# Kernel optimization log

Hardware: AMD Instinct MI355X
Metric: run time of the kernel (lower is better)

Reference implementation:

```python
import jax, jax.numpy as jnp
import numpy as np

N = 100000
F_IN = 128
E = 1_600_000
NEG_SLOPE = 0.2  # PyG GATConv default negative_slope


def _seg_sum(v, idx, n):
    return jax.ops.segment_sum(v, idx, num_segments=n)


def gcn_conv(x, W, b, src, dst, n):
    # PyG GCNConv: D^{-1/2} (A + I) D^{-1/2} X W + b (self loops already in src/dst)
    h = x @ W
    deg = _seg_sum(jnp.ones(src.shape, h.dtype), dst, n)
    dinv = jnp.where(deg > 0, jax.lax.rsqrt(deg), 0.0)
    norm = dinv[src] * dinv[dst]  # [E]
    return _seg_sum(h[src] * norm[:, None], dst, n) + b


def gat_conv(x, W, a_src, a_dst, b, src, dst, n, heads, out_ch):
    # PyG GATConv (concat=True), eval mode (dropout inactive)
    h = (x @ W).reshape(n, heads, out_ch)          # [n,H,C]
    s = jnp.einsum('nhc,hc->nh', h, a_src)          # per-node src score
    t = jnp.einsum('nhc,hc->nh', h, a_dst)          # per-node dst score
    e = jax.nn.leaky_relu(s[src] + t[dst], NEG_SLOPE)  # [E,H]
    m = jax.ops.segment_max(e, dst, num_segments=n)    # stable segment softmax
    m = jnp.where(jnp.isfinite(m), m, 0.0)
    p = jnp.exp(e - m[dst])
    denom = _seg_sum(p, dst, n)
    alpha = p / (denom[dst] + 1e-16)                 # [E,H]
    out = _seg_sum(h[src] * alpha[:, :, None], dst, n)  # [n,H,C]
    return out.reshape(n, heads * out_ch) + b


def setup_inputs():
    key = jax.random.key(0)
    ks = jax.random.split(key, 24)
    x = jax.random.normal(ks[0], (N, F_IN), jnp.float32) * 0.1
    half = N // 2
    # one-hot user/item type flags read by forward (x[:,0]==1 / x[:,1]==1)
    x = x.at[:, 0].set(0.0).at[:, 1].set(0.0)
    x = x.at[:half, 0].set(1.0).at[half:, 1].set(1.0)
    src = jax.random.randint(ks[1], (E,), 0, N, dtype=jnp.int32)
    dst = jax.random.randint(ks[2], (E,), 0, N, dtype=jnp.int32)
    edge_index = jnp.stack([src, dst])

    def p(k, shape):
        return jax.random.normal(k, shape, jnp.float32) * 0.1

    inp = {"x": x, "edge_index": edge_index,
           "gcn_w": p(ks[3], (F_IN, 16)), "gcn_b": jnp.zeros((16,), jnp.float32)}
    dims = [(16, 16, 8), (128, 16, 8), (128, 16, 8), (128, 2, 1)]
    for i, (fi, fo, h) in enumerate(dims, start=1):
        inp[f"g{i}_w"] = p(ks[3 + 4 * i], (fi, h * fo))
        inp[f"g{i}_as"] = p(ks[4 + 4 * i], (h, fo))
        inp[f"g{i}_ad"] = p(ks[5 + 4 * i], (h, fo))
        inp[f"g{i}_b"] = jnp.zeros((h * fo,), jnp.float32)
    return inp


def reference(x, edge_index, gcn_w, gcn_b,
              g1_w, g1_as, g1_ad, g1_b,
              g2_w, g2_as, g2_ad, g2_b,
              g3_w, g3_as, g3_ad, g3_b,
              g4_w, g4_as, g4_ad, g4_b):
    n = x.shape[0]
    loops = jnp.arange(n, dtype=edge_index.dtype)  # self loops (added by GCN/GAT layers)
    src = jnp.concatenate([edge_index[0], loops])
    dst = jnp.concatenate([edge_index[1], loops])
    h = jax.nn.elu(gcn_conv(x, gcn_w, gcn_b, src, dst, n))
    h = jax.nn.elu(gat_conv(h, g1_w, g1_as, g1_ad, g1_b, src, dst, n, 8, 16))
    h = jax.nn.elu(gat_conv(h, g2_w, g2_as, g2_ad, g2_b, src, dst, n, 8, 16))
    h = jax.nn.elu(gat_conv(h, g3_w, g3_as, g3_ad, g3_b, src, dst, n, 8, 16))
    h = jax.nn.elu(gat_conv(h, g4_w, g4_as, g4_ad, g4_b, src, dst, n, 1, 2))  # [n,2]
    half = n // 2  # users are rows [:half], items rows [half:]
    out = jnp.concatenate([h[:half], h[half:]], axis=1)  # [half,4]
    return jax.nn.log_softmax(out, axis=1)
```

## Files before the change

### kernel.cpp

```cpp
#include <hip/hip_runtime.h>
#include <cstddef>
#include <cstdint>

#define NN 100000
#define NPAD 100032
#define NE 1600000
#define ET (NE + NN)
#define ETP_MAX (ET + 8 * NN)
#define HALFN (NN / 2)
#define NEG_SLOPE 0.2f
#define SCB 1024
#define RP 8
#define RNODES (NN / RP)
#define CHUNK 8192

typedef __attribute__((ext_vector_type(8))) short short8v;
typedef __attribute__((ext_vector_type(4))) float float4v;
typedef __attribute__((ext_vector_type(2))) float float2v;

__device__ __forceinline__ float lrelu(float x) { return x > 0.f ? x : NEG_SLOPE * x; }

__device__ __forceinline__ uint16_t f2bf(float f) {
  uint32_t u = __float_as_uint(f);
  uint32_t r = u + 0x7fffu + ((u >> 16) & 1u);
  return (uint16_t)(r >> 16);
}
__device__ __forceinline__ float bflo(uint32_t u) { return __uint_as_float(u << 16); }
__device__ __forceinline__ float bfhi(uint32_t u) { return __uint_as_float(u & 0xffff0000u); }

template<int K, int M>
__launch_bounds__(256)
__global__ void gemm4_kernel(const float* __restrict__ X, const float* __restrict__ W,
                             float* __restrict__ Y, int n) {
  constexpr int CG = M / 4;
  constexpr int RG = 256 / CG;
  constexpr int RPT = 2;
  constexpr int RT = RG * RPT;
  constexpr int KP = K + 1;
  __shared__ __align__(16) float sW[K * M];
  __shared__ float sX[RT * KP];
  for (int i = threadIdx.x; i < K * M; i += 256) sW[i] = W[i];
  const int jg = threadIdx.x % CG;
  const int rg = threadIdx.x / CG;
  const int r0 = rg * RPT;
  for (int base = blockIdx.x * RT; base < n; base += gridDim.x * RT) {
    __syncthreads();
    const int nrows = (n - base) < RT ? (n - base) : RT;
    for (int i = threadIdx.x; i < nrows * K; i += 256) {
      int r = i / K, c = i - r * K;
      sX[r * KP + c] = X[(size_t)base * K + i];
    }
    __syncthreads();
    float acc[RPT][4];
    #pragma unroll
    for (int rr = 0; rr < RPT; ++rr) acc[rr][0] = acc[rr][1] = acc[rr][2] = acc[rr][3] = 0.f;
    #pragma unroll 4
    for (int k = 0; k < K; ++k) {
      const float4 w = *(const float4*)&sW[k * M + jg * 4];
      #pragma unroll
      for (int rr = 0; rr < RPT; ++rr) {
        const float xv = sX[(r0 + rr) * KP + k];
        acc[rr][0] = fmaf(xv, w.x, acc[rr][0]);
        acc[rr][1] = fmaf(xv, w.y, acc[rr][1]);
        acc[rr][2] = fmaf(xv, w.z, acc[rr][2]);
        acc[rr][3] = fmaf(xv, w.w, acc[rr][3]);
      }
    }
    #pragma unroll
    for (int rr = 0; rr < RPT; ++rr) {
      if (r0 + rr < nrows) {
        float4 o = make_float4(acc[rr][0], acc[rr][1], acc[rr][2], acc[rr][3]);
        *(float4*)&Y[(size_t)(base + r0 + rr) * M + jg * 4] = o;
      }
    }
  }
}

template<int KB>
__launch_bounds__(256)
__global__ void wpack_kernel(const float* __restrict__ W, uint16_t* __restrict__ wp,
                             int Kreal) {
  int tid = blockIdx.x * 256 + threadIdx.x;
  if (tid >= KB * 8 * 64) return;
  int lane = tid & 63;
  int ctkb = tid >> 6;
  int kb = ctkb % KB, ct = ctkb / KB;
  int nc = ct * 16 + (lane & 15);
  int k0 = kb * 32 + (lane >> 4) * 8;
  ushort4 o0, o1;
  uint16_t v[8];
  #pragma unroll
  for (int j = 0; j < 8; ++j) {
    int k = k0 + j;
    v[j] = (k < Kreal) ? f2bf(W[(size_t)k * 128 + nc]) : (uint16_t)0;
  }
  o0.x = v[0]; o0.y = v[1]; o0.z = v[2]; o0.w = v[3];
  o1.x = v[4]; o1.y = v[5]; o1.z = v[6]; o1.w = v[7];
  *(ushort4*)&wp[(size_t)tid * 8] = o0;
  *(ushort4*)&wp[(size_t)tid * 8 + 4] = o1;
}

template<int KB, int XS>
__launch_bounds__(256)
__global__ void gemm_mfma_kernel(const uint16_t* __restrict__ X,
                                 const uint16_t* __restrict__ wp,
                                 const float* __restrict__ aS, const float* __restrict__ aD,
                                 uint16_t* __restrict__ Y,
                                 float* __restrict__ S, float* __restrict__ T, int n) {
  __shared__ float sC[4][16 * 136];
  const int wv = threadIdx.x >> 6;
  const int lane = threadIdx.x & 63;
  const int rowbase = blockIdx.x * 64 + wv * 16;
  int arow = rowbase + (lane & 15);
  if (arow >= n) arow = n - 1;
  const uint16_t* xp = X + (size_t)arow * XS + ((lane >> 4) * 8);
  short8v a[KB];
  #pragma unroll
  for (int kb = 0; kb < KB; ++kb) a[kb] = *(const short8v*)(xp + kb * 32);
  #pragma unroll
  for (int ct = 0; ct < 8; ++ct) {
    float4v acc = {0.f, 0.f, 0.f, 0.f};
    #pragma unroll
    for (int kb = 0; kb < KB; ++kb) {
      short8v b = *(const short8v*)&wp[(size_t)((ct * KB + kb) * 64 + lane) * 8];
      acc = __builtin_amdgcn_mfma_f32_16x16x32_bf16(a[kb], b, acc, 0, 0, 0);
    }
    #pragma unroll
    for (int r = 0; r < 4; ++r)
      sC[wv][((lane >> 4) * 4 + r) * 136 + ct * 16 + (lane & 15)] = acc[r];
  }
  #pragma unroll
  for (int t = 0; t < 4; ++t) {
    int idx = t * 64 + lane;
    int row = idx >> 4;
    int c8 = idx & 15;
    const float* pr = &sC[wv][row * 136 + c8 * 8];
    float4 lo = *(const float4*)pr;
    float4 hi = *(const float4*)(pr + 4);
    uint4 o;
    o.x = (uint32_t)f2bf(lo.x) | ((uint32_t)f2bf(lo.y) << 16);
    o.y = (uint32_t)f2bf(lo.z) | ((uint32_t)f2bf(lo.w) << 16);
    o.z = (uint32_t)f2bf(hi.x) | ((uint32_t)f2bf(hi.y) << 16);
    o.w = (uint32_t)f2bf(hi.z) | ((uint32_t)f2bf(hi.w) << 16);
    *(uint4*)&Y[(size_t)(rowbase + row) * 128 + c8 * 8] = o;
  }
  {
    int r = lane & 15;
    int hg = lane >> 4;
    int node = rowbase + r;
    if (node < n) {
      #pragma unroll
      for (int hh = 0; hh < 2; ++hh) {
        int h = hg * 2 + hh;
        float sv = 0.f, tv = 0.f;
        #pragma unroll
        for (int c = 0; c < 16; ++c) {
          float v = sC[wv][r * 136 + h * 16 + c];
          sv = fmaf(v, aS[h * 16 + c], sv);
          tv = fmaf(v, aD[h * 16 + c], tv);
        }
        S[(size_t)node * 8 + h] = sv;
        T[(size_t)node * 8 + h] = tv;
      }
    }
  }
}

template<int K, int M, int ROWS>
__launch_bounds__(256)
__global__ void gemm_s_kernel(const uint16_t* __restrict__ Xb, const float* __restrict__ W,
                              float* __restrict__ Y, int n) {
  constexpr int KP = K + 1;
  __shared__ float sW[K * M];
  __shared__ float sX[ROWS * KP];
  for (int i = threadIdx.x; i < K * M; i += 256) sW[i] = W[i];
  for (int base = blockIdx.x * ROWS; base < n; base += gridDim.x * ROWS) {
    __syncthreads();
    const int nrows = (n - base) < ROWS ? (n - base) : ROWS;
    for (int i = threadIdx.x; i < nrows * (K / 4); i += 256) {
      int r = i / (K / 4), c = i - r * (K / 4);
      uint2 u = *(const uint2*)&Xb[(size_t)(base + r) * K + c * 4];
      sX[r * KP + c * 4 + 0] = bflo(u.x);
      sX[r * KP + c * 4 + 1] = bfhi(u.x);
      sX[r * KP + c * 4 + 2] = bflo(u.y);
      sX[r * KP + c * 4 + 3] = bfhi(u.y);
    }
    __syncthreads();
    for (int o = threadIdx.x; o < nrows * M; o += 256) {
      int r = o / M, j = o - r * M;
      float a = 0.f;
      #pragma unroll
      for (int k = 0; k < K; ++k) a = fmaf(sX[r * KP + k], sW[k * M + j], a);
      Y[(size_t)(base + r) * M + j] = a;
    }
  }
}

__global__ void spad_kernel(float* __restrict__ S, float* __restrict__ T) {
  if (threadIdx.x < 8) {
    S[(size_t)NN * 8 + threadIdx.x] = -1e30f;
    T[(size_t)NN * 8 + threadIdx.x] = 0.f;
  }
}

template<int H, int C>
__launch_bounds__(256)
__global__ void score_kernel(const float* __restrict__ Hm,
                             const float* __restrict__ aS, const float* __restrict__ aD,
                             float* __restrict__ S, float* __restrict__ T, int n) {
  int idx = blockIdx.x * 256 + threadIdx.x;
  int tot = n * H;
  if (idx >= tot + H) return;
  if (idx >= tot) { S[idx] = -1e30f; T[idx] = 0.f; return; }
  int h = idx & (H - 1);
  const float* hp = Hm + (size_t)idx * C;
  float s = 0.f, t = 0.f;
  #pragma unroll
  for (int c = 0; c < C; ++c) {
    float v = hp[c];
    s = fmaf(v, aS[h * C + c], s);
    t = fmaf(v, aD[h * C + c], t);
  }
  S[idx] = s;
  T[idx] = t;
}

__launch_bounds__(256)
__global__ void rank_kernel(const int* __restrict__ edst, int* __restrict__ cursor,
                            int* __restrict__ rank) {
  int e = blockIdx.x * 256 + threadIdx.x;
  if (e >= ET) return;
  int dn = e < NE ? edst[e] : e - NE;
  rank[e] = atomicAdd(&cursor[dn], 1);
}

__device__ __forceinline__ int pad8(int d) { return (d + 7) & ~7; }

__launch_bounds__(256)
__global__ void scan1_kernel(const int* __restrict__ degi, int* __restrict__ rowptr,
                             int* __restrict__ bsums) {
  __shared__ int sd[256];
  int t = threadIdx.x;
  int base = blockIdx.x * SCB + t * 4;
  int v0 = base + 0 < NN ? pad8(degi[base + 0]) : 0;
  int v1 = base + 1 < NN ? pad8(degi[base + 1]) : 0;
  int v2 = base + 2 < NN ? pad8(degi[base + 2]) : 0;
  int v3 = base + 3 < NN ? pad8(degi[base + 3]) : 0;
  int s = v0 + v1 + v2 + v3;
  sd[t] = s;
  __syncthreads();
  for (int off = 1; off < 256; off <<= 1) {
    int x = (t >= off) ? sd[t - off] : 0;
    __syncthreads();
    sd[t] += x;
    __syncthreads();
  }
  int excl = sd[t] - s;
  if (t == 255) bsums[blockIdx.x] = sd[255];
  if (base + 0 < NN) rowptr[base + 0] = excl;
  excl += v0;
  if (base + 1 < NN) rowptr[base + 1] = excl;
  excl += v1;
  if (base + 2 < NN) rowptr[base + 2] = excl;
  excl += v2;
  if (base + 3 < NN) rowptr[base + 3] = excl;
}

__launch_bounds__(256)
__global__ void scan2_kernel(int* __restrict__ bsums, int nb) {
  __shared__ int sd[256];
  int t = threadIdx.x;
  int v = t < nb ? bsums[t] : 0;
  sd[t] = v;
  __syncthreads();
  for (int off = 1; off < 256; off <<= 1) {
    int x = (t >= off) ? sd[t - off] : 0;
    __syncthreads();
    sd[t] += x;
    __syncthreads();
  }
  if (t < nb) bsums[t] = sd[t] - v;
  if (t == nb - 1) bsums[nb] = sd[t];
}

__launch_bounds__(256)
__global__ void scan3_kernel(int* __restrict__ rowptr, const int* __restrict__ bsums, int nb) {
  int i = blockIdx.x * 256 + threadIdx.x;
  if (i < NN) rowptr[i] += bsums[i / SCB];
  if (i == 0) rowptr[NN] = bsums[nb];
}

__launch_bounds__(256)
__global__ void dinv_kernel(const int* __restrict__ deg, float* __restrict__ dinv) {
  int i = blockIdx.x * 256 + threadIdx.x;
  if (i > NN) return;
  if (i == NN) { dinv[i] = 0.f; return; }
  int d = deg[i];
  dinv[i] = d > 0 ? rsqrtf((float)d) : 0.f;
}

__launch_bounds__(256)
__global__ void csr_fill_kernel(int* __restrict__ csr) {
  int i = blockIdx.x * 256 + threadIdx.x;
  if (i < ETP_MAX) csr[i] = NN;
}

__launch_bounds__(256)
__global__ void scatter_part_kernel(const int* __restrict__ esrc, const int* __restrict__ edst,
                                    const int* __restrict__ rowptr, const int* __restrict__ rank,
                                    int* __restrict__ csr_src) {
  int p = blockIdx.x & (RP - 1);
  int c = blockIdx.x >> 3;
  int lo = p * RNODES, hi = lo + RNODES;
  int e0 = c * CHUNK;
  int e1 = e0 + CHUNK < ET ? e0 + CHUNK : ET;
  for (int e = e0 + threadIdx.x; e < e1; e += 256) {
    int dn = e < NE ? edst[e] : e - NE;
    if (dn >= lo && dn < hi) {
      int sn = e < NE ? esrc[e] : e - NE;
      csr_src[rowptr[dn] + rank[e]] = sn;
    }
  }
}

__launch_bounds__(256)
__global__ void fused_gat_kernel(const int* __restrict__ rowptr, const int* __restrict__ csr,
                                 const float* __restrict__ S, const float* __restrict__ T,
                                 const uint16_t* __restrict__ Hm, const float* __restrict__ bias,
                                 uint16_t* __restrict__ Outb) {
  const int lane = threadIdx.x & 63;
  const int d = (blockIdx.x * 256 + threadIdx.x) >> 6;
  if (d >= NN) return;
  const int rs = rowptr[d];
  const int deg = rowptr[d + 1] - rs;
  const int eg = lane >> 4;
  const int cl = lane & 15;
  const int hp = cl >> 1;
  const float Th = T[(size_t)d * 8 + hp];
  const char* sb = (const char*)S;
  const char* hb = (const char*)Hm;
  float m = -1e38f;
  float s = 0.f;
  float2v A0 = {0.f, 0.f}, A1 = {0.f, 0.f}, A2 = {0.f, 0.f}, A3 = {0.f, 0.f};
  const uint32_t clo = (uint32_t)(cl << 4);
  const uint32_t hpo = (uint32_t)(hp << 2);
  int iA = rs + eg;
  int snA = csr[iA];
  int snB = csr[iA + 4];
  for (int l0 = 0; l0 < deg; l0 += 8) {
    int snA2 = csr[iA + 8];
    int snB2 = csr[iA + 12];
    uint4 uA = *(const uint4*)(hb + (((uint32_t)snA << 8) + clo));
    uint4 uB = *(const uint4*)(hb + (((uint32_t)snB << 8) + clo));
    float svA = *(const float*)(sb + (((uint32_t)snA << 5) + hpo));
    float svB = *(const float*)(sb + (((uint32_t)snB << 5) + hpo));
    iA += 8;
    float eA = lrelu(svA + Th);
    float eB = lrelu(svB + Th);
    float nm = fmaxf(m, fmaxf(eA, eB));
    if (nm > m) {
      float sc = __expf(m - nm);
      float2v scv = {sc, sc};
      s *= sc;
      A0 *= scv; A1 *= scv; A2 *= scv; A3 *= scv;
      m = nm;
    }
    float pA = __expf(eA - m);
    float pB = __expf(eB - m);
    s += pA + pB;
    float2v ppA = {pA, pA}, ppB = {pB, pB};
    A0 = ppA * (float2v){bflo(uA.x), bfhi(uA.x)} + A0;
    A1 = ppA * (float2v){bflo(uA.y), bfhi(uA.y)} + A1;
    A2 = ppA * (float2v){bflo(uA.z), bfhi(uA.z)} + A2;
    A3 = ppA * (float2v){bflo(uA.w), bfhi(uA.w)} + A3;
    A0 = ppB * (float2v){bflo(uB.x), bfhi(uB.x)} + A0;
    A1 = ppB * (float2v){bflo(uB.y), bfhi(uB.y)} + A1;
    A2 = ppB * (float2v){bflo(uB.z), bfhi(uB.z)} + A2;
    A3 = ppB * (float2v){bflo(uB.w), bfhi(uB.w)} + A3;
    snA = snA2; snB = snB2;
  }
  #pragma unroll
  for (int mask = 16; mask <= 32; mask <<= 1) {
    float om = __shfl_xor(m, mask);
    float os = __shfl_xor(s, mask);
    float o0x = __shfl_xor(A0.x, mask), o0y = __shfl_xor(A0.y, mask);
    float o1x = __shfl_xor(A1.x, mask), o1y = __shfl_xor(A1.y, mask);
    float o2x = __shfl_xor(A2.x, mask), o2y = __shfl_xor(A2.y, mask);
    float o3x = __shfl_xor(A3.x, mask), o3y = __shfl_xor(A3.y, mask);
    float nm = fmaxf(m, om);
    float s1 = __expf(m - nm), s2 = __expf(om - nm);
    s = s * s1 + os * s2;
    A0.x = A0.x * s1 + o0x * s2; A0.y = A0.y * s1 + o0y * s2;
    A1.x = A1.x * s1 + o1x * s2; A1.y = A1.y * s1 + o1y * s2;
    A2.x = A2.x * s1 + o2x * s2; A2.y = A2.y * s1 + o2y * s2;
    A3.x = A3.x * s1 + o3x * s2; A3.y = A3.y * s1 + o3y * s2;
    m = nm;
  }
  if (lane < 16) {
    const float inv = 1.f / (s + 1e-16f);
    float4 b0 = *(const float4*)&bias[cl * 8];
    float4 b1 = *(const float4*)&bias[cl * 8 + 4];
    float v0 = fmaf(A0.x, inv, b0.x), v1 = fmaf(A0.y, inv, b0.y);
    float v2 = fmaf(A1.x, inv, b0.z), v3 = fmaf(A1.y, inv, b0.w);
    float v4 = fmaf(A2.x, inv, b1.x), v5 = fmaf(A2.y, inv, b1.y);
    float v6 = fmaf(A3.x, inv, b1.z), v7 = fmaf(A3.y, inv, b1.w);
    v0 = v0 > 0.f ? v0 : expm1f(v0); v1 = v1 > 0.f ? v1 : expm1f(v1);
    v2 = v2 > 0.f ? v2 : expm1f(v2); v3 = v3 > 0.f ? v3 : expm1f(v3);
    v4 = v4 > 0.f ? v4 : expm1f(v4); v5 = v5 > 0.f ? v5 : expm1f(v5);
    v6 = v6 > 0.f ? v6 : expm1f(v6); v7 = v7 > 0.f ? v7 : expm1f(v7);
    uint4 o;
    o.x = (uint32_t)f2bf(v0) | ((uint32_t)f2bf(v1) << 16);
    o.y = (uint32_t)f2bf(v2) | ((uint32_t)f2bf(v3) << 16);
    o.z = (uint32_t)f2bf(v4) | ((uint32_t)f2bf(v5) << 16);
    o.w = (uint32_t)f2bf(v6) | ((uint32_t)f2bf(v7) << 16);
    *(uint4*)&Outb[(size_t)d * 128 + cl * 8] = o;
  }
}

__launch_bounds__(256)
__global__ void fused_gat1_kernel(const int* __restrict__ rowptr, const int* __restrict__ csr,
                                  const float* __restrict__ S, const float* __restrict__ T,
                                  const float* __restrict__ Hm2, const float* __restrict__ bias,
                                  float* __restrict__ galpha, float* __restrict__ Out) {
  int d = (blockIdx.x * 256 + threadIdx.x) >> 6;
  if (d >= NN) return;
  int lane = threadIdx.x & 63;
  int rs = rowptr[d], deg = rowptr[d + 1] - rs;
  float Td = T[d];
  int sn = 0;
  float e = -1e30f;
  if (lane < deg) { sn = csr[rs + lane]; e = lrelu(S[sn] + Td); }
  float m = e;
  for (int l2 = 64 + lane; l2 < deg; l2 += 64) {
    float e2 = lrelu(S[csr[rs + l2]] + Td);
    galpha[rs + l2] = e2;
    m = fmaxf(m, e2);
  }
  #pragma unroll
  for (int mask = 1; mask < 64; mask <<= 1) m = fmaxf(m, __shfl_xor(m, mask));
  float p = (lane < deg) ? __expf(e - m) : 0.f;
  float sum = p;
  for (int l2 = 64 + lane; l2 < deg; l2 += 64) {
    float p2 = __expf(galpha[rs + l2] - m);
    galpha[rs + l2] = p2;
    sum += p2;
  }
  #pragma unroll
  for (int mask = 1; mask < 64; mask <<= 1) sum += __shfl_xor(sum, mask);
  float inv = 1.f / (sum + 1e-16f);
  float a0 = 0.f, a1 = 0.f;
  if (lane < deg) {
    float2 hv = *(const float2*)&Hm2[(size_t)sn * 2];
    a0 = p * hv.x; a1 = p * hv.y;
  }
  for (int l2 = 64 + lane; l2 < deg; l2 += 64) {
    int sn2 = csr[rs + l2];
    float p2 = galpha[rs + l2];
    float2 hv = *(const float2*)&Hm2[(size_t)sn2 * 2];
    a0 = fmaf(p2, hv.x, a0); a1 = fmaf(p2, hv.y, a1);
  }
  #pragma unroll
  for (int mask = 1; mask < 64; mask <<= 1) {
    a0 += __shfl_xor(a0, mask); a1 += __shfl_xor(a1, mask);
  }
  if (lane == 0) {
    float v0 = fmaf(a0, inv, bias[0]);
    float v1 = fmaf(a1, inv, bias[1]);
    v0 = v0 > 0.f ? v0 : expm1f(v0);
    v1 = v1 > 0.f ? v1 : expm1f(v1);
    float2 o; o.x = v0; o.y = v1;
    *(float2*)&Out[(size_t)d * 2] = o;
  }
}

__launch_bounds__(256)
__global__ void gcn_pull_kernel(const int* __restrict__ rowptr, const int* __restrict__ csr_src,
                                const float* __restrict__ dinv, const float* __restrict__ Hm,
                                const float* __restrict__ bias, uint16_t* __restrict__ Outb) {
  int d = blockIdx.x * 16 + threadIdx.x / 16;
  if (d >= NN) return;
  int f = threadIdx.x & 15;
  int rs = rowptr[d], re = rowptr[d + 1];
  float acc = 0.f;
  int j = rs;
  for (; j + 4 <= re; j += 4) {
    int s0 = csr_src[j], s1 = csr_src[j + 1], s2 = csr_src[j + 2], s3 = csr_src[j + 3];
    float d0 = dinv[s0], d1 = dinv[s1], d2 = dinv[s2], d3 = dinv[s3];
    float h0 = Hm[(size_t)s0 * 16 + f], h1 = Hm[(size_t)s1 * 16 + f];
    float h2 = Hm[(size_t)s2 * 16 + f], h3 = Hm[(size_t)s3 * 16 + f];
    acc = fmaf(d0, h0, acc); acc = fmaf(d1, h1, acc);
    acc = fmaf(d2, h2, acc); acc = fmaf(d3, h3, acc);
  }
  for (; j < re; ++j) {
    int sn = csr_src[j];
    acc = fmaf(dinv[sn], Hm[(size_t)sn * 16 + f], acc);
  }
  float v = acc * dinv[d] + bias[f];
  v = v > 0.f ? v : expm1f(v);
  Outb[(size_t)d * 32 + f] = f2bf(v);
  Outb[(size_t)d * 32 + 16 + f] = 0;
}

__launch_bounds__(256)
__global__ void final_kernel(const float* __restrict__ A, float* __restrict__ Out) {
  int i = blockIdx.x * 256 + threadIdx.x;
  if (i >= HALFN) return;
  float v0 = A[(size_t)i * 2 + 0];
  float v1 = A[(size_t)i * 2 + 1];
  float v2 = A[(size_t)(i + HALFN) * 2 + 0];
  float v3 = A[(size_t)(i + HALFN) * 2 + 1];
  float m = fmaxf(fmaxf(v0, v1), fmaxf(v2, v3));
  float e0 = __expf(v0 - m), e1 = __expf(v1 - m), e2 = __expf(v2 - m), e3 = __expf(v3 - m);
  float l = logf(e0 + e1 + e2 + e3) + m;
  Out[(size_t)i * 4 + 0] = v0 - l;
  Out[(size_t)i * 4 + 1] = v1 - l;
  Out[(size_t)i * 4 + 2] = v2 - l;
  Out[(size_t)i * 4 + 3] = v3 - l;
}

extern "C" void kernel_launch(void* const* d_in, const int* in_sizes, int n_in,
                              void* d_out, int out_size, void* d_ws, size_t ws_size,
                              hipStream_t stream) {
  const float* x     = (const float*)d_in[0];
  const int*   eidx  = (const int*)d_in[1];
  const int*   esrc  = eidx;
  const int*   edst  = eidx + NE;
  const float* gcn_w = (const float*)d_in[2];
  const float* gcn_b = (const float*)d_in[3];

  char* ws = (char*)d_ws;
  uint16_t* hbf    = (uint16_t*)(ws + 0);
  uint16_t* bufAb  = (uint16_t*)(ws + 25700000);
  uint16_t* gcnHbf = (uint16_t*)(ws + 51400000);
  float*    bufB   = (float*)   (ws + 57900000);
  float*    bufC   = (float*)   (ws + 64400000);
  float*    Sb     = (float*)   (ws + 65300000);
  float*    Tb     = (float*)   (ws + 68600000);
  float*    galpha = (float*)   (ws + 71900000);
  int*      rowptr = (int*)     (ws + 151900000);
  int*      cursor = (int*)     (ws + 152300008);
  int*      csr    = (int*)     (ws + 152700008);
  float*    dinv   = (float*)   (ws + 162700008);
  int*      bsums  = (int*)     (ws + 163100016);
  int*      rank   = (int*)     (ws + 163100528);
  uint16_t* wpck   = (uint16_t*)(ws + 169900528);

  constexpr int NB_SCAN = (NN + SCB - 1) / SCB;

  hipMemsetAsync(cursor, 0, (size_t)NN * 4, stream);
  rank_kernel<<<(ET + 255) / 256, 256, 0, stream>>>(edst, cursor, rank);
  scan1_kernel<<<NB_SCAN, 256, 0, stream>>>(cursor, rowptr, bsums);
  scan2_kernel<<<1, 256, 0, stream>>>(bsums, NB_SCAN);
  scan3_kernel<<<(NN + 256) / 256, 256, 0, stream>>>(rowptr, bsums, NB_SCAN);
  dinv_kernel<<<(NN + 256) / 256, 256, 0, stream>>>(cursor, dinv);
  csr_fill_kernel<<<(ETP_MAX + 255) / 256, 256, 0, stream>>>(csr);
  {
    int nch = (ET + CHUNK - 1) / CHUNK;
    scatter_part_kernel<<<nch * RP, 256, 0, stream>>>(esrc, edst, rowptr, rank, csr);
  }
  spad_kernel<<<1, 64, 0, stream>>>(Sb, Tb);

  {
    int tiles = (NN + 127) / 128;
    if (tiles > 4096) tiles = 4096;
    gemm4_kernel<128, 16><<<tiles, 256, 0, stream>>>(x, gcn_w, bufB, NN);
  }
  gcn_pull_kernel<<<(NN + 15) / 16, 256, 0, stream>>>(rowptr, csr, dinv, bufB, gcn_b, gcnHbf);

  wpack_kernel<1><<<2, 256, 0, stream>>>((const float*)d_in[4], wpck, 16);
  gemm_mfma_kernel<1, 32><<<NPAD / 64, 256, 0, stream>>>(
      gcnHbf, wpck, (const float*)d_in[5], (const float*)d_in[6], hbf, Sb, Tb, NN);
  fused_gat_kernel<<<(NN * 64 + 255) / 256, 256, 0, stream>>>(
      rowptr, csr, Sb, Tb, hbf, (const float*)d_in[7], bufAb);

  wpack_kernel<4><<<8, 256, 0, stream>>>((const float*)d_in[8], wpck, 128);
  gemm_mfma_kernel<4, 128><<<NPAD / 64, 256, 0, stream>>>(
      bufAb, wpck, (const float*)d_in[9], (const float*)d_in[10], hbf, Sb, Tb, NN);
  fused_gat_kernel<<<(NN * 64 + 255) / 256, 256, 0, stream>>>(
      rowptr, csr, Sb, Tb, hbf, (const float*)d_in[11], bufAb);

  wpack_kernel<4><<<8, 256, 0, stream>>>((const float*)d_in[12], wpck, 128);
  gemm_mfma_kernel<4, 128><<<NPAD / 64, 256, 0, stream>>>(
      bufAb, wpck, (const float*)d_in[13], (const float*)d_in[14], hbf, Sb, Tb, NN);
  fused_gat_kernel<<<(NN * 64 + 255) / 256, 256, 0, stream>>>(
      rowptr, csr, Sb, Tb, hbf, (const float*)d_in[15], bufAb);

  {
    int tiles = (NN + 127) / 128;
    if (tiles > 2048) tiles = 2048;
    gemm_s_kernel<128, 2, 128><<<tiles, 256, 0, stream>>>(
        bufAb, (const float*)d_in[16], bufB, NN);
    score_kernel<1, 2><<<(NN + 1 + 255) / 256, 256, 0, stream>>>(
        bufB, (const float*)d_in[17], (const float*)d_in[18], Sb, Tb, NN);
    fused_gat1_kernel<<<(NN * 64 + 255) / 256, 256, 0, stream>>>(
        rowptr, csr, Sb, Tb, bufB, (const float*)d_in[19], galpha, bufC);
  }

  final_kernel<<<(HALFN + 255) / 256, 256, 0, stream>>>(bufC, (float*)d_out);
}
```

Before: 542.9 us.

## Fuse final-layer scores into GEMM, online-softmax GAT1, trim CSR padding fill

The last layer's small GEMM now also computes the attention scores, which removes the separate score kernel. The separate pad-sentinel kernel is dropped: the GEMM writes the layer-1 sentinels and the dinv kernel writes the 8-head ones. The final GAT layer switches from a three-pass softmax with a galpha scratch buffer to a single-pass online softmax, using 16 lanes per destination node so each wavefront handles 4 nodes. The full CSR sentinel fill is replaced by filling only each row's padding slots. The wide GAT epilogue now has all 64 lanes store 2 values each instead of 16 lanes storing 8. The per-row padding loop can diverge, and 16-lane rows may underuse lanes when a node has few edges.

```diff
diff --git a/kernel.cpp b/kernel.cpp
--- a/kernel.cpp
+++ b/kernel.cpp
@@ -166,14 +166,21 @@
   }
 }
 
-template<int K, int M, int ROWS>
-__launch_bounds__(256)
-__global__ void gemm_s_kernel(const uint16_t* __restrict__ Xb, const float* __restrict__ W,
-                              float* __restrict__ Y, int n) {
+template<int K, int ROWS>
+__launch_bounds__(256)
+__global__ void gemm_s2_kernel(const uint16_t* __restrict__ Xb, const float* __restrict__ W,
+                               const float* __restrict__ aS, const float* __restrict__ aD,
+                               float* __restrict__ Y, float* __restrict__ S,
+                               float* __restrict__ T, int n) {
   constexpr int KP = K + 1;
-  __shared__ float sW[K * M];
+  __shared__ float sW[K * 2];
   __shared__ float sX[ROWS * KP];
-  for (int i = threadIdx.x; i < K * M; i += 256) sW[i] = W[i];
+  if (blockIdx.x == 0 && threadIdx.x == 0) {
+    S[NN] = -1e30f; T[NN] = 0.f;
+    Y[(size_t)NN * 2] = 0.f; Y[(size_t)NN * 2 + 1] = 0.f;
+  }
+  for (int i = threadIdx.x; i < K * 2; i += 256) sW[i] = W[i];
+  const float as0 = aS[0], as1 = aS[1], ad0 = aD[0], ad1 = aD[1];
   for (int base = blockIdx.x * ROWS; base < n; base += gridDim.x * ROWS) {
     __syncthreads();
     const int nrows = (n - base) < ROWS ? (n - base) : ROWS;
@@ -186,43 +193,21 @@
       sX[r * KP + c * 4 + 3] = bfhi(u.y);
     }
     __syncthreads();
-    for (int o = threadIdx.x; o < nrows * M; o += 256) {
-      int r = o / M, j = o - r * M;
-      float a = 0.f;
-      #pragma unroll
-      for (int k = 0; k < K; ++k) a = fmaf(sX[r * KP + k], sW[k * M + j], a);
-      Y[(size_t)(base + r) * M + j] = a;
-    }
-  }
-}
-
-__global__ void spad_kernel(float* __restrict__ S, float* __restrict__ T) {
-  if (threadIdx.x < 8) {
-    S[(size_t)NN * 8 + threadIdx.x] = -1e30f;
-    T[(size_t)NN * 8 + threadIdx.x] = 0.f;
-  }
-}
-
-template<int H, int C>
-__launch_bounds__(256)
-__global__ void score_kernel(const float* __restrict__ Hm,
-                             const float* __restrict__ aS, const float* __restrict__ aD,
-                             float* __restrict__ S, float* __restrict__ T, int n) {
-  int idx = blockIdx.x * 256 + threadIdx.x;
-  int tot = n * H;
-  if (idx >= tot + H) return;
-  if (idx >= tot) { S[idx] = -1e30f; T[idx] = 0.f; return; }
-  int h = idx & (H - 1);
-  const float* hp = Hm + (size_t)idx * C;
-  float s = 0.f, t = 0.f;
-  #pragma unroll
-  for (int c = 0; c < C; ++c) {
-    float v = hp[c];
-    s = fmaf(v, aS[h * C + c], s);
-    t = fmaf(v, aD[h * C + c], t);
-  }
-  S[idx] = s;
-  T[idx] = t;
+    for (int r = threadIdx.x; r < nrows; r += 256) {
+      float a0 = 0.f, a1 = 0.f;
+      #pragma unroll 4
+      for (int k = 0; k < K; ++k) {
+        float xv = sX[r * KP + k];
+        a0 = fmaf(xv, sW[k * 2], a0);
+        a1 = fmaf(xv, sW[k * 2 + 1], a1);
+      }
+      int node = base + r;
+      float2 o; o.x = a0; o.y = a1;
+      *(float2*)&Y[(size_t)node * 2] = o;
+      S[node] = a0 * as0 + a1 * as1;
+      T[node] = a0 * ad0 + a1 * ad1;
+    }
+  }
 }
 
 __launch_bounds__(256)
@@ -291,18 +276,30 @@
 }
 
 __launch_bounds__(256)
-__global__ void dinv_kernel(const int* __restrict__ deg, float* __restrict__ dinv) {
+__global__ void dinv_kernel(const int* __restrict__ deg, float* __restrict__ dinv,
+                            float* __restrict__ S8, float* __restrict__ T8) {
   int i = blockIdx.x * 256 + threadIdx.x;
   if (i > NN) return;
-  if (i == NN) { dinv[i] = 0.f; return; }
+  if (i == NN) {
+    dinv[i] = 0.f;
+    #pragma unroll
+    for (int h = 0; h < 8; ++h) {
+      S8[(size_t)NN * 8 + h] = -1e30f;
+      T8[(size_t)NN * 8 + h] = 0.f;
+    }
+    return;
+  }
   int d = deg[i];
   dinv[i] = d > 0 ? rsqrtf((float)d) : 0.f;
 }
 
 __launch_bounds__(256)
-__global__ void csr_fill_kernel(int* __restrict__ csr) {
+__global__ void padfill_kernel(const int* __restrict__ rowptr, const int* __restrict__ deg,
+                               int* __restrict__ csr) {
   int i = blockIdx.x * 256 + threadIdx.x;
-  if (i < ETP_MAX) csr[i] = NN;
+  if (i >= NN) return;
+  int e = rowptr[i] + deg[i], e1 = rowptr[i + 1];
+  for (; e < e1; ++e) csr[e] = NN;
 }
 
 __launch_bounds__(256)
@@ -396,24 +393,18 @@
     A3.x = A3.x * s1 + o3x * s2; A3.y = A3.y * s1 + o3y * s2;
     m = nm;
   }
-  if (lane < 16) {
+  {
+    float2v Blo = (eg & 1) ? A1 : A0;
+    float2v Bhi = (eg & 1) ? A3 : A2;
+    float2v B = (eg & 2) ? Bhi : Blo;
     const float inv = 1.f / (s + 1e-16f);
-    float4 b0 = *(const float4*)&bias[cl * 8];
-    float4 b1 = *(const float4*)&bias[cl * 8 + 4];
-    float v0 = fmaf(A0.x, inv, b0.x), v1 = fmaf(A0.y, inv, b0.y);
-    float v2 = fmaf(A1.x, inv, b0.z), v3 = fmaf(A1.y, inv, b0.w);
-    float v4 = fmaf(A2.x, inv, b1.x), v5 = fmaf(A2.y, inv, b1.y);
-    float v6 = fmaf(A3.x, inv, b1.z), v7 = fmaf(A3.y, inv, b1.w);
-    v0 = v0 > 0.f ? v0 : expm1f(v0); v1 = v1 > 0.f ? v1 : expm1f(v1);
-    v2 = v2 > 0.f ? v2 : expm1f(v2); v3 = v3 > 0.f ? v3 : expm1f(v3);
-    v4 = v4 > 0.f ? v4 : expm1f(v4); v5 = v5 > 0.f ? v5 : expm1f(v5);
-    v6 = v6 > 0.f ? v6 : expm1f(v6); v7 = v7 > 0.f ? v7 : expm1f(v7);
-    uint4 o;
-    o.x = (uint32_t)f2bf(v0) | ((uint32_t)f2bf(v1) << 16);
-    o.y = (uint32_t)f2bf(v2) | ((uint32_t)f2bf(v3) << 16);
-    o.z = (uint32_t)f2bf(v4) | ((uint32_t)f2bf(v5) << 16);
-    o.w = (uint32_t)f2bf(v6) | ((uint32_t)f2bf(v7) << 16);
-    *(uint4*)&Outb[(size_t)d * 128 + cl * 8] = o;
+    float2 b = *(const float2*)&bias[cl * 8 + eg * 2];
+    float v0 = fmaf(B.x, inv, b.x);
+    float v1 = fmaf(B.y, inv, b.y);
+    v0 = v0 > 0.f ? v0 : expm1f(v0);
+    v1 = v1 > 0.f ? v1 : expm1f(v1);
+    uint32_t o = (uint32_t)f2bf(v0) | ((uint32_t)f2bf(v1) << 16);
+    *(uint32_t*)&Outb[(size_t)d * 128 + cl * 8 + eg * 2] = o;
   }
 }
 
@@ -421,49 +412,44 @@
 __global__ void fused_gat1_kernel(const int* __restrict__ rowptr, const int* __restrict__ csr,
                                   const float* __restrict__ S, const float* __restrict__ T,
                                   const float* __restrict__ Hm2, const float* __restrict__ bias,
-                                  float* __restrict__ galpha, float* __restrict__ Out) {
-  int d = (blockIdx.x * 256 + threadIdx.x) >> 6;
+                                  float* __restrict__ Out) {
+  int lane = threadIdx.x & 63;
+  int sub = lane >> 4, l16 = lane & 15;
+  int d = ((blockIdx.x * 256 + threadIdx.x) >> 6) * 4 + sub;
   if (d >= NN) return;
-  int lane = threadIdx.x & 63;
   int rs = rowptr[d], deg = rowptr[d + 1] - rs;
   float Td = T[d];
-  int sn = 0;
-  float e = -1e30f;
-  if (lane < deg) { sn = csr[rs + lane]; e = lrelu(S[sn] + Td); }
-  float m = e;
-  for (int l2 = 64 + lane; l2 < deg; l2 += 64) {
-    float e2 = lrelu(S[csr[rs + l2]] + Td);
-    galpha[rs + l2] = e2;
-    m = fmaxf(m, e2);
+  float m = -1e38f, sAcc = 0.f, a0 = 0.f, a1 = 0.f;
+  for (int l = l16; l < deg; l += 16) {
+    int sn = csr[rs + l];
+    float2 hv = *(const float2*)&Hm2[(size_t)sn * 2];
+    float sv = S[sn];
+    float e = lrelu(sv + Td);
+    float nm = fmaxf(m, e);
+    if (e > m) {
+      float sc = __expf(m - nm);
+      sAcc *= sc; a0 *= sc; a1 *= sc; m = nm;
+    }
+    float p = __expf(e - m);
+    sAcc += p;
+    a0 = fmaf(p, hv.x, a0);
+    a1 = fmaf(p, hv.y, a1);
   }
   #pragma unroll
-  for (int mask = 1; mask < 64; mask <<= 1) m = fmaxf(m, __shfl_xor(m, mask));
-  float p = (lane < deg) ? __expf(e - m) : 0.f;
-  float sum = p;
-  for (int l2 = 64 + lane; l2 < deg; l2 += 64) {
-    float p2 = __expf(galpha[rs + l2] - m);
-    galpha[rs + l2] = p2;
-    sum += p2;
-  }
-  #pragma unroll
-  for (int mask = 1; mask < 64; mask <<= 1) sum += __shfl_xor(sum, mask);
-  float inv = 1.f / (sum + 1e-16f);
-  float a0 = 0.f, a1 = 0.f;
-  if (lane < deg) {
-    float2 hv = *(const float2*)&Hm2[(size_t)sn * 2];
-    a0 = p * hv.x; a1 = p * hv.y;
-  }
-  for (int l2 = 64 + lane; l2 < deg; l2 += 64) {
-    int sn2 = csr[rs + l2];
-    float p2 = galpha[rs + l2];
-    float2 hv = *(const float2*)&Hm2[(size_t)sn2 * 2];
-    a0 = fmaf(p2, hv.x, a0); a1 = fmaf(p2, hv.y, a1);
-  }
-  #pragma unroll
-  for (int mask = 1; mask < 64; mask <<= 1) {
-    a0 += __shfl_xor(a0, mask); a1 += __shfl_xor(a1, mask);
-  }
-  if (lane == 0) {
+  for (int mask = 1; mask <= 8; mask <<= 1) {
+    float om = __shfl_xor(m, mask);
+    float os = __shfl_xor(sAcc, mask);
+    float oa0 = __shfl_xor(a0, mask);
+    float oa1 = __shfl_xor(a1, mask);
+    float nm = fmaxf(m, om);
+    float s1 = __expf(m - nm), s2 = __expf(om - nm);
+    sAcc = sAcc * s1 + os * s2;
+    a0 = a0 * s1 + oa0 * s2;
+    a1 = a1 * s1 + oa1 * s2;
+    m = nm;
+  }
+  if (l16 == 0) {
+    float inv = 1.f / (sAcc + 1e-16f);
     float v0 = fmaf(a0, inv, bias[0]);
     float v1 = fmaf(a1, inv, bias[1]);
     v0 = v0 > 0.f ? v0 : expm1f(v0);
@@ -536,7 +522,6 @@
   float*    bufC   = (float*)   (ws + 64400000);
   float*    Sb     = (float*)   (ws + 65300000);
   float*    Tb     = (float*)   (ws + 68600000);
-  float*    galpha = (float*)   (ws + 71900000);
   int*      rowptr = (int*)     (ws + 151900000);
   int*      cursor = (int*)     (ws + 152300008);
   int*      csr    = (int*)     (ws + 152700008);
@@ -552,13 +537,12 @@
   scan1_kernel<<<NB_SCAN, 256, 0, stream>>>(cursor, rowptr, bsums);
   scan2_kernel<<<1, 256, 0, stream>>>(bsums, NB_SCAN);
   scan3_kernel<<<(NN + 256) / 256, 256, 0, stream>>>(rowptr, bsums, NB_SCAN);
-  dinv_kernel<<<(NN + 256) / 256, 256, 0, stream>>>(cursor, dinv);
-  csr_fill_kernel<<<(ETP_MAX + 255) / 256, 256, 0, stream>>>(csr);
+  dinv_kernel<<<(NN + 256) / 256, 256, 0, stream>>>(cursor, dinv, Sb, Tb);
+  padfill_kernel<<<(NN + 255) / 256, 256, 0, stream>>>(rowptr, cursor, csr);
   {
     int nch = (ET + CHUNK - 1) / CHUNK;
     scatter_part_kernel<<<nch * RP, 256, 0, stream>>>(esrc, edst, rowptr, rank, csr);
   }
-  spad_kernel<<<1, 64, 0, stream>>>(Sb, Tb);
 
   {
     int tiles = (NN + 127) / 128;
@@ -588,12 +572,11 @@
   {
     int tiles = (NN + 127) / 128;
     if (tiles > 2048) tiles = 2048;
-    gemm_s_kernel<128, 2, 128><<<tiles, 256, 0, stream>>>(
-        bufAb, (const float*)d_in[16], bufB, NN);
-    score_kernel<1, 2><<<(NN + 1 + 255) / 256, 256, 0, stream>>>(
-        bufB, (const float*)d_in[17], (const float*)d_in[18], Sb, Tb, NN);
-    fused_gat1_kernel<<<(NN * 64 + 255) / 256, 256, 0, stream>>>(
-        rowptr, csr, Sb, Tb, bufB, (const float*)d_in[19], galpha, bufC);
+    gemm_s2_kernel<128, 128><<<tiles, 256, 0, stream>>>(
+        bufAb, (const float*)d_in[16], (const float*)d_in[17], (const float*)d_in[18],
+        bufB, Sb, Tb, NN);
+    fused_gat1_kernel<<<(NN * 16 + 255) / 256, 256, 0, stream>>>(
+        rowptr, csr, Sb, Tb, bufB, (const float*)d_in[19], bufC);
   }
 
   final_kernel<<<(HALFN + 255) / 256, 256, 0, stream>>>(bufC, (float*)d_out);
```

After: 518.4 us. 1.05x faster.
